# Optimization experiments

Measured on AMD Instinct MI355X. Metric: run time of the kernel, lower is better.

## Reference

```python
import jax, jax.numpy as jnp
import numpy as np

N, K, D_IN, D_H, D_A, N_CLS = 8192, 10, 1024, 512, 256, 4


def setup_inputs() -> dict:
    key = jax.random.key(0)
    ks = jax.random.split(key, 20)
    def lin(k, fan_in, shape):
        return jax.random.normal(k, shape, dtype=jnp.float32) / np.sqrt(fan_in)
    return {
        "x_path": jax.random.normal(ks[0], (N, D_IN), dtype=jnp.float32),
        "cluster_id": jax.random.randint(ks[1], (N,), 0, K),
        # per-cluster phi MLP (Linear 1024->512, ReLU, Linear 512->512, ReLU); dropout = eval identity
        "W1": lin(ks[2], D_IN, (K, D_IN, D_H)), "b1": jnp.zeros((K, D_H), jnp.float32),
        "W2": lin(ks[3], D_H, (K, D_H, D_H)), "b2": jnp.zeros((K, D_H), jnp.float32),
        # attention_net fc: Linear 512->512 + ReLU
        "fc_W": lin(ks[4], D_H, (D_H, D_H)), "fc_b": jnp.zeros((D_H,), jnp.float32),
        # Attn_Net_Gated: a=tanh(Va), b=sigmoid(Vb), A=(a*b)@Vc
        "Va": lin(ks[5], D_H, (D_H, D_A)), "ba": jnp.zeros((D_A,), jnp.float32),
        "Vb": lin(ks[6], D_H, (D_H, D_A)), "bb": jnp.zeros((D_A,), jnp.float32),
        "Vc": lin(ks[7], D_A, (D_A, 1)), "bc": jnp.zeros((1,), jnp.float32),
        # rho: Linear 512->256 + ReLU
        "rho_W": lin(ks[8], D_H, (D_H, D_A)), "rho_b": jnp.zeros((D_A,), jnp.float32),
        # classifier: Linear 256->4
        "cls_W": lin(ks[9], D_A, (D_A, N_CLS)), "cls_b": jnp.zeros((N_CLS,), jnp.float32),
    }


def reference(x_path, cluster_id, W1, b1, W2, b2, fc_W, fc_b,
              Va, ba, Vb, bb, Vc, bc, rho_W, rho_b, cls_W, cls_b):
    # mask[k, n] = 1 if patch n belongs to cluster k
    mask = (cluster_id[None, :] == jnp.arange(K)[:, None]).astype(x_path.dtype)  # [K, N]

    # per-cluster 2-layer MLP applied to all patches, masked mean-pool (= AdaptiveAvgPool1d(1))
    def phi(W1i, b1i, W2i, b2i):
        h = jax.nn.relu(x_path @ W1i + b1i)          # [N, 512]
        return jax.nn.relu(h @ W2i + b2i)            # [N, 512]
    y = jax.vmap(phi)(W1, b1, W2, b2)                # [K, N, 512]
    cnt = mask.sum(axis=1)                           # [K]
    pooled = jnp.einsum('kn,knd->kd', mask, y) / jnp.maximum(cnt, 1.0)[:, None]  # [K, 512]
    # empty cluster -> zeros (matches torch.zeros((1,512)) branch since b terms are zero via where)
    pooled = jnp.where(cnt[:, None] > 0, pooled, 0.0)

    # attention_net: fc + gated attention
    h = jax.nn.relu(pooled @ fc_W + fc_b)            # [K, 512]
    a = jnp.tanh(h @ Va + ba)                        # [K, 256]
    b = jax.nn.sigmoid(h @ Vb + bb)                  # [K, 256]
    A = (a * b) @ Vc + bc                            # [K, 1]
    A = jax.nn.softmax(A.T, axis=1)                  # [1, K]
    h_path = A @ h                                   # [1, 512]
    h_path = jax.nn.relu(h_path @ rho_W + rho_b)[0]  # [256]
    logits = (h_path @ cls_W + cls_b)[None, :]       # [1, 4]
    Y_hat = jnp.argmax(logits, axis=1, keepdims=True)
    hazards = jax.nn.sigmoid(logits)
    S = jnp.cumprod(1.0 - hazards, axis=1)
    return hazards, S, Y_hat
```

## Files before the change

kernel.cpp:

```cpp
#include <hip/hip_runtime.h>
#include <math.h>

#define NPATCH 8192
#define KC     10
#define DIN    1024
#define DH     512
#define DA     256
#define NCLS   4

#define TM  32
#define LDA 520

typedef unsigned short u16;
typedef short bf16x8 __attribute__((ext_vector_type(8)));
typedef float f32x4  __attribute__((ext_vector_type(4)));

#define OFF_CNT   0
#define OFF_IDX   64
#define OFF_PSUM  327744
#define OFF_H     348224
#define OFF_S     368704
#define OFF_H2    368768
#define OFF_W1P   369792
#define OFF_W2P   10855552
#define OFF_XB    16098432
#define OFF_H1    32875648

__device__ __forceinline__ u16 f2bf(float f) {
  union { float f; unsigned u; } v; v.f = f;
  unsigned r = (v.u + 0x7fffu + ((v.u >> 16) & 1u)) >> 16;
  return (u16)r;
}

struct __align__(8) U16x4 { u16 x, y, z, w; };

__device__ __forceinline__ void async16(const void* gp, void* lp) {
  __builtin_amdgcn_global_load_lds(
      (const __attribute__((address_space(1))) void*)gp,
      (__attribute__((address_space(3))) void*)lp, 16, 0, 0);
}

#define W1_TILES (KC * (DIN / 32) * (DH / 32))
#define W2_TILES (KC * (DH / 32) * (DH / 32))
#define NB_BUCKET 32
#define NB_XB     2048
#define NB_PREP   (NB_BUCKET + W1_TILES + W2_TILES + NB_XB)

__global__ __launch_bounds__(256) void prep_kernel(
    const int* __restrict__ cid, int* __restrict__ cnt,
    int* __restrict__ idxlist, const float* __restrict__ W1,
    const float* __restrict__ W2, u16* __restrict__ W1p,
    u16* __restrict__ W2p, const float* __restrict__ x,
    u16* __restrict__ xb, float* __restrict__ psum,
    float* __restrict__ sstore) {
  int b = blockIdx.x, t = threadIdx.x;
  if (b < NB_BUCKET) {
    int g = b * 256 + t;
    if (g < KC * DH) psum[g] = 0.f;
    if (g < KC) sstore[g] = 0.f;
    __shared__ int lcnt[KC], lbase[KC];
    if (t < KC) lcnt[t] = 0;
    __syncthreads();
    int n = b * 256 + t;
    int k = cid[n];
    int myoff = atomicAdd(&lcnt[k], 1);
    __syncthreads();
    if (t < KC) lbase[t] = atomicAdd(&cnt[t], lcnt[t]);
    __syncthreads();
    idxlist[k * NPATCH + lbase[k] + myoff] = n;
  } else if (b < NB_BUCKET + W1_TILES + W2_TILES) {
    __shared__ u16 tile[32][33];
    int bb = b - NB_BUCKET;
    const float* src;
    u16* dst;
    if (bb < W1_TILES) {
      int k = bb / 512, rem = bb % 512;
      int kb = rem / 16, n0 = (rem % 16) * 32;
      src = W1 + (size_t)k * DIN * DH + (size_t)kb * 32 * DH + n0;
      dst = W1p + (((size_t)(k * 32 + kb) * 512 + n0) * 32);
    } else {
      int b2 = bb - W1_TILES;
      int k = b2 / 256, rem = b2 % 256;
      int kb = rem / 16, n0 = (rem % 16) * 32;
      src = W2 + (size_t)k * DH * DH + (size_t)kb * 32 * DH + n0;
      dst = W2p + (((size_t)(k * 16 + kb) * 512 + n0) * 32);
    }
    {
      int ki = t >> 3, n4 = (t & 7) * 4;
      float4 v = *(const float4*)&src[(size_t)ki * DH + n4];
      tile[ki][n4 + 0] = f2bf(v.x);
      tile[ki][n4 + 1] = f2bf(v.y);
      tile[ki][n4 + 2] = f2bf(v.z);
      tile[ki][n4 + 3] = f2bf(v.w);
    }
    __syncthreads();
    {
      int n = t >> 3, ki = (t & 7) * 4;
      U16x4 o = {tile[ki + 0][n], tile[ki + 1][n], tile[ki + 2][n],
                 tile[ki + 3][n]};
      *(U16x4*)&dst[(size_t)n * 32 + ki] = o;
    }
  } else {
    int cb = b - (NB_BUCKET + W1_TILES + W2_TILES);
    size_t basei = (size_t)cb * 4096;
#pragma unroll
    for (int i = 0; i < 4; ++i) {
      size_t off = basei + (size_t)i * 1024 + (size_t)t * 4;
      float4 v = *(const float4*)(x + off);
      U16x4 o = {f2bf(v.x), f2bf(v.y), f2bf(v.z), f2bf(v.w)};
      *(U16x4*)(xb + off) = o;
    }
  }
}

__global__ __launch_bounds__(256) void phi1_kernel(
    const u16* __restrict__ xb, const u16* __restrict__ W1p,
    const float* __restrict__ b1, const int* __restrict__ cnt,
    const int* __restrict__ idxlist, u16* __restrict__ h1) {
  const int k = blockIdx.y;
  const int base = blockIdx.x * TM;
  const int nq = blockIdx.z;
  const int cntk = cnt[k];
  if (base >= cntk) return;

  const int tid = threadIdx.x;
  const int w = tid >> 6, lane = tid & 63;
  const int quad = lane >> 4, l16 = lane & 15;

  __shared__ __align__(16) u16 A_sh[TM * LDA];
  __shared__ int ridx[TM];
  if (tid < TM) {
    int r = base + tid;
    ridx[tid] = (r < cntk) ? idxlist[k * NPATCH + r] : -1;
  }
  __syncthreads();

  const f32x4 zero4 = {0.f, 0.f, 0.f, 0.f};
  f32x4 acc[2][2];
#pragma unroll
  for (int m = 0; m < 2; ++m)
#pragma unroll
    for (int nt = 0; nt < 2; ++nt) acc[m][nt] = zero4;

  for (int kh = 0; kh < 2; ++kh) {
    if (kh) __syncthreads();
    for (int rr = 0; rr < 8; ++rr) {
      int r = w * 8 + rr;
      int src = ridx[r];
      if (src >= 0) {
        async16(xb + (size_t)src * DIN + kh * 512 + lane * 8, &A_sh[r * LDA]);
      } else {
        bf16x8 z = {0, 0, 0, 0, 0, 0, 0, 0};
        *(bf16x8*)&A_sh[r * LDA + lane * 8] = z;
      }
    }
    __syncthreads();

    const u16* wb = W1p + ((size_t)(k * 32 + kh * 16) * 512 +
                           (nq * 128 + w * 32 + l16)) * 32 + quad * 8;
    bf16x8 B[2][8];
#pragma unroll
    for (int s = 0; s < 4; ++s)
#pragma unroll
      for (int nt = 0; nt < 2; ++nt)
        B[0][s * 2 + nt] = *(const bf16x8*)(wb + (size_t)s * 16384 + nt * 512);
#pragma unroll
    for (int g = 0; g < 4; ++g) {
      const int cur = g & 1, nxt = cur ^ 1;
      if (g < 3) {
#pragma unroll
        for (int s = 0; s < 4; ++s)
#pragma unroll
          for (int nt = 0; nt < 2; ++nt)
            B[nxt][s * 2 + nt] = *(const bf16x8*)(
                wb + (size_t)((g + 1) * 4 + s) * 16384 + nt * 512);
      }
#pragma unroll
      for (int s = 0; s < 4; ++s) {
        const int ks = g * 4 + s;
        bf16x8 af0 = *(const bf16x8*)&A_sh[l16 * LDA + ks * 32 + quad * 8];
        bf16x8 af1 =
            *(const bf16x8*)&A_sh[(16 + l16) * LDA + ks * 32 + quad * 8];
#pragma unroll
        for (int nt = 0; nt < 2; ++nt) {
          acc[0][nt] = __builtin_amdgcn_mfma_f32_16x16x32_bf16(
              af0, B[cur][s * 2 + nt], acc[0][nt], 0, 0, 0);
          acc[1][nt] = __builtin_amdgcn_mfma_f32_16x16x32_bf16(
              af1, B[cur][s * 2 + nt], acc[1][nt], 0, 0, 0);
        }
      }
    }
  }

  __syncthreads();
#pragma unroll
  for (int m = 0; m < 2; ++m)
#pragma unroll
    for (int nt = 0; nt < 2; ++nt) {
      int c = w * 32 + nt * 16 + l16;
      float bias = b1[k * DH + nq * 128 + c];
#pragma unroll
      for (int r = 0; r < 4; ++r) {
        int row = m * 16 + quad * 4 + r;
        A_sh[row * 136 + c] = f2bf(fmaxf(acc[m][nt][r] + bias, 0.f));
      }
    }
  __syncthreads();
  {
    int row = tid >> 3, seg = tid & 7;
    int n = ridx[row];
    if (n >= 0) {
      u16* dst = h1 + (size_t)n * DH + nq * 128 + seg * 16;
#pragma unroll
      for (int j = 0; j < 2; ++j)
        *(bf16x8*)(dst + j * 8) =
            *(const bf16x8*)&A_sh[row * 136 + seg * 16 + j * 8];
    }
  }
}

__global__ __launch_bounds__(256) void phi2_kernel(
    const u16* __restrict__ h1, const u16* __restrict__ W2p,
    const float* __restrict__ b2, const int* __restrict__ cnt,
    const int* __restrict__ idxlist, float* __restrict__ psum) {
  const int k = blockIdx.y;
  const int base = blockIdx.x * TM;
  const int nq = blockIdx.z;
  const int cntk = cnt[k];
  if (base >= cntk) return;

  const int tid = threadIdx.x;
  const int w = tid >> 6, lane = tid & 63;
  const int quad = lane >> 4, l16 = lane & 15;

  __shared__ __align__(16) u16 H_sh[TM * LDA];
  __shared__ int ridx[TM];
  if (tid < TM) {
    int r = base + tid;
    ridx[tid] = (r < cntk) ? idxlist[k * NPATCH + r] : -1;
  }
  __syncthreads();

  for (int rr = 0; rr < 8; ++rr) {
    int r = w * 8 + rr;
    int src = ridx[r];
    if (src >= 0) {
      async16(h1 + (size_t)src * DH + lane * 8, &H_sh[r * LDA]);
    } else {
      bf16x8 z = {0, 0, 0, 0, 0, 0, 0, 0};
      *(bf16x8*)&H_sh[r * LDA + lane * 8] = z;
    }
  }
  __syncthreads();

  const f32x4 zero4 = {0.f, 0.f, 0.f, 0.f};
  f32x4 acc[2][2];
#pragma unroll
  for (int m = 0; m < 2; ++m)
#pragma unroll
    for (int nt = 0; nt < 2; ++nt) acc[m][nt] = zero4;

  const u16* wb = W2p + ((size_t)(k * 16) * 512 +
                         (nq * 128 + w * 32 + l16)) * 32 + quad * 8;
  bf16x8 B[2][8];
#pragma unroll
  for (int s = 0; s < 4; ++s)
#pragma unroll
    for (int nt = 0; nt < 2; ++nt)
      B[0][s * 2 + nt] = *(const bf16x8*)(wb + (size_t)s * 16384 + nt * 512);
#pragma unroll
  for (int g = 0; g < 4; ++g) {
    const int cur = g & 1, nxt = cur ^ 1;
    if (g < 3) {
#pragma unroll
      for (int s = 0; s < 4; ++s)
#pragma unroll
        for (int nt = 0; nt < 2; ++nt)
          B[nxt][s * 2 + nt] = *(const bf16x8*)(
              wb + (size_t)((g + 1) * 4 + s) * 16384 + nt * 512);
    }
#pragma unroll
    for (int s = 0; s < 4; ++s) {
      const int ks = g * 4 + s;
      bf16x8 af0 = *(const bf16x8*)&H_sh[l16 * LDA + ks * 32 + quad * 8];
      bf16x8 af1 =
          *(const bf16x8*)&H_sh[(16 + l16) * LDA + ks * 32 + quad * 8];
#pragma unroll
      for (int nt = 0; nt < 2; ++nt) {
        acc[0][nt] = __builtin_amdgcn_mfma_f32_16x16x32_bf16(
            af0, B[cur][s * 2 + nt], acc[0][nt], 0, 0, 0);
        acc[1][nt] = __builtin_amdgcn_mfma_f32_16x16x32_bf16(
            af1, B[cur][s * 2 + nt], acc[1][nt], 0, 0, 0);
      }
    }
  }

  float vmask[2][4];
#pragma unroll
  for (int m = 0; m < 2; ++m)
#pragma unroll
    for (int r = 0; r < 4; ++r)
      vmask[m][r] = (ridx[m * 16 + quad * 4 + r] >= 0) ? 1.f : 0.f;

#pragma unroll
  for (int nt = 0; nt < 2; ++nt) {
    int col = nq * 128 + w * 32 + nt * 16 + l16;
    float bias = b2[k * DH + col];
    float s = 0.f;
#pragma unroll
    for (int m = 0; m < 2; ++m)
#pragma unroll
      for (int r = 0; r < 4; ++r)
        s += vmask[m][r] * fmaxf(acc[m][nt][r] + bias, 0.f);
    s += __shfl_xor(s, 16, 64);
    s += __shfl_xor(s, 32, 64);
    if (quad == 0) atomicAdd(&psum[k * DH + col], s);
  }
}

__global__ __launch_bounds__(256) void fc_kernel(
    const float* __restrict__ psum, const int* __restrict__ cnt,
    const float* __restrict__ fcW, const float* __restrict__ fcb,
    float* __restrict__ hstore) {
  __shared__ float p_sh[KC * DH];
  __shared__ float invs[16];
  __shared__ float red[16 * 16 * KC];
  const int tid = threadIdx.x;
  const int j0 = blockIdx.x * 16;
  const int j = tid & 15, dq = tid >> 4;

  if (tid < KC) {
    int c = cnt[tid];
    invs[tid] = (c > 0) ? 1.f / (float)c : 0.f;
  }
  __syncthreads();
#pragma unroll
  for (int it = 0; it < KC * DH / 256; ++it) {
    int e = it * 256 + tid;
    p_sh[e] = psum[e] * invs[e >> 9];
  }
  __syncthreads();

  float acc[KC];
#pragma unroll
  for (int k = 0; k < KC; ++k) acc[k] = 0.f;
#pragma unroll 8
  for (int i = 0; i < 32; ++i) {
    int ii = (i + dq) & 31;
    int d = dq * 32 + ii;
    float wv = fcW[(size_t)d * DH + j0 + j];
#pragma unroll
    for (int k = 0; k < KC; ++k)
      acc[k] = fmaf(p_sh[k * DH + d], wv, acc[k]);
  }
#pragma unroll
  for (int k = 0; k < KC; ++k) red[(dq * 16 + j) * KC + k] = acc[k];
  __syncthreads();
  if (tid < 16 * KC) {
    int jj = tid / KC, k = tid % KC;
    float s = 0.f;
#pragma unroll
    for (int q = 0; q < 16; ++q) s += red[(q * 16 + jj) * KC + k];
    hstore[k * DH + j0 + jj] = fmaxf(s + fcb[j0 + jj], 0.f);
  }
}

__global__ __launch_bounds__(256) void attn_kernel(
    const float* __restrict__ hstore, const float* __restrict__ Va,
    const float* __restrict__ ba, const float* __restrict__ Vb,
    const float* __restrict__ bb_, const float* __restrict__ Vc,
    float* __restrict__ sstore) {
  __shared__ float h_sh[KC * DH];
  __shared__ float reda[16 * 16 * KC];
  __shared__ float redb[16 * 16 * KC];
  __shared__ float gred[16 * KC];
  const int tid = threadIdx.x;
  const int j0 = blockIdx.x * 16;
  const int j = tid & 15, dq = tid >> 4;

#pragma unroll
  for (int it = 0; it < KC * DH / 256; ++it) {
    int e = it * 256 + tid;
    h_sh[e] = hstore[e];
  }
  __syncthreads();

  float sa[KC], sb[KC];
#pragma unroll
  for (int k = 0; k < KC; ++k) { sa[k] = 0.f; sb[k] = 0.f; }
#pragma unroll 8
  for (int i = 0; i < 32; ++i) {
    int ii = (i + dq) & 31;
    int d = dq * 32 + ii;
    float va = Va[(size_t)d * DA + j0 + j];
    float vb = Vb[(size_t)d * DA + j0 + j];
#pragma unroll
    for (int k = 0; k < KC; ++k) {
      float h = h_sh[k * DH + d];
      sa[k] = fmaf(h, va, sa[k]);
      sb[k] = fmaf(h, vb, sb[k]);
    }
  }
#pragma unroll
  for (int k = 0; k < KC; ++k) {
    reda[(dq * 16 + j) * KC + k] = sa[k];
    redb[(dq * 16 + j) * KC + k] = sb[k];
  }
  __syncthreads();
  if (tid < 16 * KC) {
    int jj = tid / KC, k = tid % KC;
    float ta = 0.f, tb = 0.f;
#pragma unroll
    for (int q = 0; q < 16; ++q) {
      ta += reda[(q * 16 + jj) * KC + k];
      tb += redb[(q * 16 + jj) * KC + k];
    }
    float a = tanhf(ta + ba[j0 + jj]);
    float b = 1.f / (1.f + expf(-(tb + bb_[j0 + jj])));
    gred[jj * KC + k] = a * b * Vc[j0 + jj];
  }
  __syncthreads();
  if (tid < KC) {
    float s = 0.f;
#pragma unroll
    for (int jj = 0; jj < 16; ++jj) s += gred[jj * KC + tid];
    atomicAdd(&sstore[tid], s);
  }
}

__global__ __launch_bounds__(256) void rho_kernel(
    const float* __restrict__ hstore, const float* __restrict__ sstore,
    const float* __restrict__ rhoW, const float* __restrict__ rhob,
    float* __restrict__ h2g) {
  __shared__ float ws_sh[KC];
  __shared__ float hp_sh[DH];
  __shared__ float red[8 * 32];
  const int tid = threadIdx.x;
  const int j0 = blockIdx.x * 32;
  const int j = tid & 31, dq = tid >> 5;

  if (tid == 0) {
    float sv[KC], m = -1e30f;
#pragma unroll
    for (int k = 0; k < KC; ++k) { sv[k] = sstore[k]; m = fmaxf(m, sv[k]); }
    float Z = 0.f;
#pragma unroll
    for (int k = 0; k < KC; ++k) { sv[k] = expf(sv[k] - m); Z += sv[k]; }
    float invZ = 1.f / Z;
#pragma unroll
    for (int k = 0; k < KC; ++k) ws_sh[k] = sv[k] * invZ;
  }
  __syncthreads();
#pragma unroll
  for (int it = 0; it < 2; ++it) {
    int d = it * 256 + tid;
    float s = 0.f;
#pragma unroll
    for (int k = 0; k < KC; ++k) s = fmaf(ws_sh[k], hstore[k * DH + d], s);
    hp_sh[d] = s;
  }
  __syncthreads();

  float acc = 0.f;
#pragma unroll 8
  for (int i = 0; i < 64; ++i) {
    int d = dq * 64 + i;
    acc = fmaf(hp_sh[d], rhoW[(size_t)d * DA + j0 + j], acc);
  }
  red[dq * 32 + j] = acc;
  __syncthreads();
  if (tid < 32) {
    float s = 0.f;
#pragma unroll
    for (int q = 0; q < 8; ++q) s += red[q * 32 + tid];
    h2g[j0 + tid] = fmaxf(s + rhob[j0 + tid], 0.f);
  }
}

__global__ __launch_bounds__(256) void cls_kernel(
    const float* __restrict__ h2g, const float* __restrict__ clsW,
    const float* __restrict__ clsb, float* __restrict__ out) {
  __shared__ float rd[NCLS][256];
  const int tid = threadIdx.x;
  float h = h2g[tid];
#pragma unroll
  for (int c = 0; c < NCLS; ++c) rd[c][tid] = h * clsW[tid * NCLS + c];
  __syncthreads();
  for (int s = 128; s > 0; s >>= 1) {
    if (tid < s) {
#pragma unroll
      for (int c = 0; c < NCLS; ++c) rd[c][tid] += rd[c][tid + s];
    }
    __syncthreads();
  }
  if (tid == 0) {
    float lg[NCLS], hz[NCLS];
    int best = 0;
#pragma unroll
    for (int c = 0; c < NCLS; ++c) {
      lg[c] = rd[c][0] + clsb[c];
      hz[c] = 1.f / (1.f + expf(-lg[c]));
      if (lg[c] > lg[best]) best = c;
    }
    float S = 1.f;
#pragma unroll
    for (int c = 0; c < NCLS; ++c) out[c] = hz[c];
#pragma unroll
    for (int c = 0; c < NCLS; ++c) {
      S *= (1.f - hz[c]);
      out[NCLS + c] = S;
    }
    out[2 * NCLS] = (float)best;
  }
}

extern "C" void kernel_launch(void* const* d_in, const int* in_sizes, int n_in,
                              void* d_out, int out_size, void* d_ws,
                              size_t ws_size, hipStream_t stream) {
  const float* x    = (const float*)d_in[0];
  const int*   cid  = (const int*)d_in[1];
  const float* W1   = (const float*)d_in[2];
  const float* b1   = (const float*)d_in[3];
  const float* W2   = (const float*)d_in[4];
  const float* b2   = (const float*)d_in[5];
  const float* fcW  = (const float*)d_in[6];
  const float* fcb  = (const float*)d_in[7];
  const float* Va   = (const float*)d_in[8];
  const float* ba   = (const float*)d_in[9];
  const float* Vb   = (const float*)d_in[10];
  const float* bb_  = (const float*)d_in[11];
  const float* Vc   = (const float*)d_in[12];
  const float* rhoW = (const float*)d_in[14];
  const float* rhob = (const float*)d_in[15];
  const float* clsW = (const float*)d_in[16];
  const float* clsb = (const float*)d_in[17];
  float* out = (float*)d_out;

  char* ws = (char*)d_ws;
  int*   cnt     = (int*)(ws + OFF_CNT);
  int*   idxlist = (int*)(ws + OFF_IDX);
  float* psum    = (float*)(ws + OFF_PSUM);
  float* hstore  = (float*)(ws + OFF_H);
  float* sstore  = (float*)(ws + OFF_S);
  float* h2g     = (float*)(ws + OFF_H2);
  u16*   W1p     = (u16*)(ws + OFF_W1P);
  u16*   W2p     = (u16*)(ws + OFF_W2P);
  u16*   xb      = (u16*)(ws + OFF_XB);
  u16*   h1      = (u16*)(ws + OFF_H1);

  (void)hipMemsetAsync(cnt, 0, 64, stream);
  prep_kernel<<<NB_PREP, 256, 0, stream>>>(cid, cnt, idxlist, W1, W2, W1p, W2p,
                                           x, xb, psum, sstore);
  phi1_kernel<<<dim3(NPATCH / TM, KC, 4), 256, 0, stream>>>(xb, W1p, b1, cnt,
                                                            idxlist, h1);
  phi2_kernel<<<dim3(NPATCH / TM, KC, 4), 256, 0, stream>>>(h1, W2p, b2, cnt,
                                                            idxlist, psum);
  fc_kernel<<<32, 256, 0, stream>>>(psum, cnt, fcW, fcb, hstore);
  attn_kernel<<<16, 256, 0, stream>>>(hstore, Va, ba, Vb, bb_, Vc, sstore);
  rho_kernel<<<8, 256, 0, stream>>>(hstore, sstore, rhoW, rhob, h2g);
  cls_kernel<<<1, 256, 0, stream>>>(h2g, clsW, clsb, out);
}
```

Before: 202.2 us.

## Fuse x bf16 conversion into phi1 and merge head kernels with grid barriers

Removes the separate pass converting x to bf16; phi1 now loads fp32 rows of gathered patches and converts them to bf16 while staging into LDS. The four small tail kernels (fc, attention, rho, classifier) are merged into one 32-block kernel separated by atomic grid barriers. This targets the extra memory traffic of the conversion pass and the launch overhead of the tail kernels. The cost is that phi1 reads fp32 x (twice the bytes) once per column quarter and loses async LDS loads, and the spin barrier relies on all 32 blocks being co-resident.

```diff
diff --git a/kernel.cpp b/kernel.cpp
--- a/kernel.cpp
+++ b/kernel.cpp
@@ -16,6 +16,7 @@
 typedef float f32x4  __attribute__((ext_vector_type(4)));
 
 #define OFF_CNT   0
+#define OFF_BAR   40
 #define OFF_IDX   64
 #define OFF_PSUM  327744
 #define OFF_H     348224
@@ -23,8 +24,7 @@
 #define OFF_H2    368768
 #define OFF_W1P   369792
 #define OFF_W2P   10855552
-#define OFF_XB    16098432
-#define OFF_H1    32875648
+#define OFF_H1    16098432
 
 __device__ __forceinline__ u16 f2bf(float f) {
   union { float f; unsigned u; } v; v.f = f;
@@ -43,15 +43,13 @@
 #define W1_TILES (KC * (DIN / 32) * (DH / 32))
 #define W2_TILES (KC * (DH / 32) * (DH / 32))
 #define NB_BUCKET 32
-#define NB_XB     2048
-#define NB_PREP   (NB_BUCKET + W1_TILES + W2_TILES + NB_XB)
+#define NB_PREP   (NB_BUCKET + W1_TILES + W2_TILES)
 
 __global__ __launch_bounds__(256) void prep_kernel(
     const int* __restrict__ cid, int* __restrict__ cnt,
     int* __restrict__ idxlist, const float* __restrict__ W1,
     const float* __restrict__ W2, u16* __restrict__ W1p,
-    u16* __restrict__ W2p, const float* __restrict__ x,
-    u16* __restrict__ xb, float* __restrict__ psum,
+    u16* __restrict__ W2p, float* __restrict__ psum,
     float* __restrict__ sstore) {
   int b = blockIdx.x, t = threadIdx.x;
   if (b < NB_BUCKET) {
@@ -68,7 +66,7 @@
     if (t < KC) lbase[t] = atomicAdd(&cnt[t], lcnt[t]);
     __syncthreads();
     idxlist[k * NPATCH + lbase[k] + myoff] = n;
-  } else if (b < NB_BUCKET + W1_TILES + W2_TILES) {
+  } else {
     __shared__ u16 tile[32][33];
     int bb = b - NB_BUCKET;
     const float* src;
@@ -100,21 +98,11 @@
                  tile[ki + 3][n]};
       *(U16x4*)&dst[(size_t)n * 32 + ki] = o;
     }
-  } else {
-    int cb = b - (NB_BUCKET + W1_TILES + W2_TILES);
-    size_t basei = (size_t)cb * 4096;
-#pragma unroll
-    for (int i = 0; i < 4; ++i) {
-      size_t off = basei + (size_t)i * 1024 + (size_t)t * 4;
-      float4 v = *(const float4*)(x + off);
-      U16x4 o = {f2bf(v.x), f2bf(v.y), f2bf(v.z), f2bf(v.w)};
-      *(U16x4*)(xb + off) = o;
-    }
   }
 }
 
 __global__ __launch_bounds__(256) void phi1_kernel(
-    const u16* __restrict__ xb, const u16* __restrict__ W1p,
+    const float* __restrict__ x, const u16* __restrict__ W1p,
     const float* __restrict__ b1, const int* __restrict__ cnt,
     const int* __restrict__ idxlist, u16* __restrict__ h1) {
   const int k = blockIdx.y;
@@ -142,17 +130,25 @@
 #pragma unroll
     for (int nt = 0; nt < 2; ++nt) acc[m][nt] = zero4;
 
+  const int srow = tid >> 3;
+  const int sc0 = (tid & 7) * 4;
+  const int asrc = ridx[srow];
+
   for (int kh = 0; kh < 2; ++kh) {
     if (kh) __syncthreads();
-    for (int rr = 0; rr < 8; ++rr) {
-      int r = w * 8 + rr;
-      int src = ridx[r];
-      if (src >= 0) {
-        async16(xb + (size_t)src * DIN + kh * 512 + lane * 8, &A_sh[r * LDA]);
-      } else {
-        bf16x8 z = {0, 0, 0, 0, 0, 0, 0, 0};
-        *(bf16x8*)&A_sh[r * LDA + lane * 8] = z;
-      }
+    if (asrc >= 0) {
+      const float* xr = x + (size_t)asrc * DIN + kh * 512;
+#pragma unroll
+      for (int c = 0; c < 16; ++c) {
+        float4 v = *(const float4*)(xr + sc0 + c * 32);
+        U16x4 o = {f2bf(v.x), f2bf(v.y), f2bf(v.z), f2bf(v.w)};
+        *(U16x4*)&A_sh[srow * LDA + sc0 + c * 32] = o;
+      }
+    } else {
+      U16x4 o = {0, 0, 0, 0};
+#pragma unroll
+      for (int c = 0; c < 16; ++c)
+        *(U16x4*)&A_sh[srow * LDA + sc0 + c * 32] = o;
     }
     __syncthreads();
 
@@ -318,199 +314,210 @@
   }
 }
 
-__global__ __launch_bounds__(256) void fc_kernel(
+__device__ __forceinline__ void gsync(int* bar) {
+  __syncthreads();
+  if (threadIdx.x == 0) {
+    __threadfence();
+    atomicAdd(bar, 1);
+    while (__hip_atomic_load(bar, __ATOMIC_RELAXED,
+                             __HIP_MEMORY_SCOPE_AGENT) < 32) {
+      __builtin_amdgcn_s_sleep(1);
+    }
+    __threadfence();
+  }
+  __syncthreads();
+}
+
+__global__ __launch_bounds__(256) void head_kernel(
     const float* __restrict__ psum, const int* __restrict__ cnt,
     const float* __restrict__ fcW, const float* __restrict__ fcb,
-    float* __restrict__ hstore) {
-  __shared__ float p_sh[KC * DH];
-  __shared__ float invs[16];
-  __shared__ float red[16 * 16 * KC];
+    const float* __restrict__ Va, const float* __restrict__ ba,
+    const float* __restrict__ Vb, const float* __restrict__ bb_,
+    const float* __restrict__ Vc, const float* __restrict__ rhoW,
+    const float* __restrict__ rhob, const float* __restrict__ clsW,
+    const float* __restrict__ clsb, float* __restrict__ hstore,
+    float* __restrict__ sstore, float* __restrict__ h2g, int* __restrict__ bar,
+    float* __restrict__ out) {
+  __shared__ __align__(16) float smem[10496];
   const int tid = threadIdx.x;
-  const int j0 = blockIdx.x * 16;
-  const int j = tid & 15, dq = tid >> 4;
-
-  if (tid < KC) {
-    int c = cnt[tid];
-    invs[tid] = (c > 0) ? 1.f / (float)c : 0.f;
-  }
-  __syncthreads();
-#pragma unroll
-  for (int it = 0; it < KC * DH / 256; ++it) {
-    int e = it * 256 + tid;
-    p_sh[e] = psum[e] * invs[e >> 9];
-  }
-  __syncthreads();
-
-  float acc[KC];
-#pragma unroll
-  for (int k = 0; k < KC; ++k) acc[k] = 0.f;
+  const int blk = blockIdx.x;
+
+  {
+    float* p_sh = smem;
+    float* red = smem + 5120;
+    float* invs = smem + 7680;
+    const int j0 = blk * 16;
+    const int j = tid & 15, dq = tid >> 4;
+    if (tid < KC) {
+      int c = cnt[tid];
+      invs[tid] = (c > 0) ? 1.f / (float)c : 0.f;
+    }
+    __syncthreads();
+#pragma unroll
+    for (int it = 0; it < KC * DH / 256; ++it) {
+      int e = it * 256 + tid;
+      p_sh[e] = psum[e] * invs[e >> 9];
+    }
+    __syncthreads();
+    float acc[KC];
+#pragma unroll
+    for (int k = 0; k < KC; ++k) acc[k] = 0.f;
 #pragma unroll 8
-  for (int i = 0; i < 32; ++i) {
-    int ii = (i + dq) & 31;
-    int d = dq * 32 + ii;
-    float wv = fcW[(size_t)d * DH + j0 + j];
-#pragma unroll
-    for (int k = 0; k < KC; ++k)
-      acc[k] = fmaf(p_sh[k * DH + d], wv, acc[k]);
-  }
-#pragma unroll
-  for (int k = 0; k < KC; ++k) red[(dq * 16 + j) * KC + k] = acc[k];
-  __syncthreads();
-  if (tid < 16 * KC) {
-    int jj = tid / KC, k = tid % KC;
-    float s = 0.f;
-#pragma unroll
-    for (int q = 0; q < 16; ++q) s += red[(q * 16 + jj) * KC + k];
-    hstore[k * DH + j0 + jj] = fmaxf(s + fcb[j0 + jj], 0.f);
-  }
-}
-
-__global__ __launch_bounds__(256) void attn_kernel(
-    const float* __restrict__ hstore, const float* __restrict__ Va,
-    const float* __restrict__ ba, const float* __restrict__ Vb,
-    const float* __restrict__ bb_, const float* __restrict__ Vc,
-    float* __restrict__ sstore) {
-  __shared__ float h_sh[KC * DH];
-  __shared__ float reda[16 * 16 * KC];
-  __shared__ float redb[16 * 16 * KC];
-  __shared__ float gred[16 * KC];
-  const int tid = threadIdx.x;
-  const int j0 = blockIdx.x * 16;
-  const int j = tid & 15, dq = tid >> 4;
-
-#pragma unroll
-  for (int it = 0; it < KC * DH / 256; ++it) {
-    int e = it * 256 + tid;
-    h_sh[e] = hstore[e];
-  }
-  __syncthreads();
-
-  float sa[KC], sb[KC];
-#pragma unroll
-  for (int k = 0; k < KC; ++k) { sa[k] = 0.f; sb[k] = 0.f; }
+    for (int i = 0; i < 32; ++i) {
+      int ii = (i + dq) & 31;
+      int d = dq * 32 + ii;
+      float wv = fcW[(size_t)d * DH + j0 + j];
+#pragma unroll
+      for (int k = 0; k < KC; ++k)
+        acc[k] = fmaf(p_sh[k * DH + d], wv, acc[k]);
+    }
+#pragma unroll
+    for (int k = 0; k < KC; ++k) red[(dq * 16 + j) * KC + k] = acc[k];
+    __syncthreads();
+    if (tid < 16 * KC) {
+      int jj = tid / KC, k = tid % KC;
+      float s = 0.f;
+#pragma unroll
+      for (int q = 0; q < 16; ++q) s += red[(q * 16 + jj) * KC + k];
+      hstore[k * DH + j0 + jj] = fmaxf(s + fcb[j0 + jj], 0.f);
+    }
+  }
+  gsync(&bar[0]);
+
+  if (blk < 16) {
+    float* h_sh = smem;
+    float* reda = smem + 5120;
+    float* redb = smem + 7680;
+    float* gred = smem + 10240;
+    const int j0 = blk * 16;
+    const int j = tid & 15, dq = tid >> 4;
+#pragma unroll
+    for (int it = 0; it < KC * DH / 256; ++it) {
+      int e = it * 256 + tid;
+      h_sh[e] = hstore[e];
+    }
+    __syncthreads();
+    float sa[KC], sb[KC];
+#pragma unroll
+    for (int k = 0; k < KC; ++k) { sa[k] = 0.f; sb[k] = 0.f; }
 #pragma unroll 8
-  for (int i = 0; i < 32; ++i) {
-    int ii = (i + dq) & 31;
-    int d = dq * 32 + ii;
-    float va = Va[(size_t)d * DA + j0 + j];
-    float vb = Vb[(size_t)d * DA + j0 + j];
+    for (int i = 0; i < 32; ++i) {
+      int ii = (i + dq) & 31;
+      int d = dq * 32 + ii;
+      float va = Va[(size_t)d * DA + j0 + j];
+      float vb = Vb[(size_t)d * DA + j0 + j];
+#pragma unroll
+      for (int k = 0; k < KC; ++k) {
+        float h = h_sh[k * DH + d];
+        sa[k] = fmaf(h, va, sa[k]);
+        sb[k] = fmaf(h, vb, sb[k]);
+      }
+    }
 #pragma unroll
     for (int k = 0; k < KC; ++k) {
-      float h = h_sh[k * DH + d];
-      sa[k] = fmaf(h, va, sa[k]);
-      sb[k] = fmaf(h, vb, sb[k]);
-    }
-  }
-#pragma unroll
-  for (int k = 0; k < KC; ++k) {
-    reda[(dq * 16 + j) * KC + k] = sa[k];
-    redb[(dq * 16 + j) * KC + k] = sb[k];
-  }
-  __syncthreads();
-  if (tid < 16 * KC) {
-    int jj = tid / KC, k = tid % KC;
-    float ta = 0.f, tb = 0.f;
-#pragma unroll
-    for (int q = 0; q < 16; ++q) {
-      ta += reda[(q * 16 + jj) * KC + k];
-      tb += redb[(q * 16 + jj) * KC + k];
-    }
-    float a = tanhf(ta + ba[j0 + jj]);
-    float b = 1.f / (1.f + expf(-(tb + bb_[j0 + jj])));
-    gred[jj * KC + k] = a * b * Vc[j0 + jj];
-  }
-  __syncthreads();
-  if (tid < KC) {
-    float s = 0.f;
-#pragma unroll
-    for (int jj = 0; jj < 16; ++jj) s += gred[jj * KC + tid];
-    atomicAdd(&sstore[tid], s);
-  }
-}
-
-__global__ __launch_bounds__(256) void rho_kernel(
-    const float* __restrict__ hstore, const float* __restrict__ sstore,
-    const float* __restrict__ rhoW, const float* __restrict__ rhob,
-    float* __restrict__ h2g) {
-  __shared__ float ws_sh[KC];
-  __shared__ float hp_sh[DH];
-  __shared__ float red[8 * 32];
-  const int tid = threadIdx.x;
-  const int j0 = blockIdx.x * 32;
-  const int j = tid & 31, dq = tid >> 5;
-
-  if (tid == 0) {
-    float sv[KC], m = -1e30f;
-#pragma unroll
-    for (int k = 0; k < KC; ++k) { sv[k] = sstore[k]; m = fmaxf(m, sv[k]); }
-    float Z = 0.f;
-#pragma unroll
-    for (int k = 0; k < KC; ++k) { sv[k] = expf(sv[k] - m); Z += sv[k]; }
-    float invZ = 1.f / Z;
-#pragma unroll
-    for (int k = 0; k < KC; ++k) ws_sh[k] = sv[k] * invZ;
-  }
-  __syncthreads();
-#pragma unroll
-  for (int it = 0; it < 2; ++it) {
-    int d = it * 256 + tid;
-    float s = 0.f;
-#pragma unroll
-    for (int k = 0; k < KC; ++k) s = fmaf(ws_sh[k], hstore[k * DH + d], s);
-    hp_sh[d] = s;
-  }
-  __syncthreads();
-
-  float acc = 0.f;
+      reda[(dq * 16 + j) * KC + k] = sa[k];
+      redb[(dq * 16 + j) * KC + k] = sb[k];
+    }
+    __syncthreads();
+    if (tid < 16 * KC) {
+      int jj = tid / KC, k = tid % KC;
+      float ta = 0.f, tb = 0.f;
+#pragma unroll
+      for (int q = 0; q < 16; ++q) {
+        ta += reda[(q * 16 + jj) * KC + k];
+        tb += redb[(q * 16 + jj) * KC + k];
+      }
+      float a = tanhf(ta + ba[j0 + jj]);
+      float b = 1.f / (1.f + expf(-(tb + bb_[j0 + jj])));
+      gred[jj * KC + k] = a * b * Vc[j0 + jj];
+    }
+    __syncthreads();
+    if (tid < KC) {
+      float s = 0.f;
+#pragma unroll
+      for (int jj = 0; jj < 16; ++jj) s += gred[jj * KC + tid];
+      atomicAdd(&sstore[tid], s);
+    }
+  }
+  gsync(&bar[1]);
+
+  if (blk < 8) {
+    float* ws_sh = smem;
+    float* hp_sh = smem + 64;
+    float* red = smem + 1024;
+    const int j0 = blk * 32;
+    const int j = tid & 31, dq = tid >> 5;
+    if (tid == 0) {
+      float sv[KC], m = -1e30f;
+#pragma unroll
+      for (int k = 0; k < KC; ++k) { sv[k] = sstore[k]; m = fmaxf(m, sv[k]); }
+      float Z = 0.f;
+#pragma unroll
+      for (int k = 0; k < KC; ++k) { sv[k] = expf(sv[k] - m); Z += sv[k]; }
+      float invZ = 1.f / Z;
+#pragma unroll
+      for (int k = 0; k < KC; ++k) ws_sh[k] = sv[k] * invZ;
+    }
+    __syncthreads();
+#pragma unroll
+    for (int it = 0; it < 2; ++it) {
+      int d = it * 256 + tid;
+      float s = 0.f;
+#pragma unroll
+      for (int k = 0; k < KC; ++k) s = fmaf(ws_sh[k], hstore[k * DH + d], s);
+      hp_sh[d] = s;
+    }
+    __syncthreads();
+    float acc = 0.f;
 #pragma unroll 8
-  for (int i = 0; i < 64; ++i) {
-    int d = dq * 64 + i;
-    acc = fmaf(hp_sh[d], rhoW[(size_t)d * DA + j0 + j], acc);
-  }
-  red[dq * 32 + j] = acc;
-  __syncthreads();
-  if (tid < 32) {
-    float s = 0.f;
-#pragma unroll
-    for (int q = 0; q < 8; ++q) s += red[q * 32 + tid];
-    h2g[j0 + tid] = fmaxf(s + rhob[j0 + tid], 0.f);
-  }
-}
-
-__global__ __launch_bounds__(256) void cls_kernel(
-    const float* __restrict__ h2g, const float* __restrict__ clsW,
-    const float* __restrict__ clsb, float* __restrict__ out) {
-  __shared__ float rd[NCLS][256];
-  const int tid = threadIdx.x;
-  float h = h2g[tid];
-#pragma unroll
-  for (int c = 0; c < NCLS; ++c) rd[c][tid] = h * clsW[tid * NCLS + c];
-  __syncthreads();
-  for (int s = 128; s > 0; s >>= 1) {
-    if (tid < s) {
-#pragma unroll
-      for (int c = 0; c < NCLS; ++c) rd[c][tid] += rd[c][tid + s];
-    }
-    __syncthreads();
-  }
-  if (tid == 0) {
-    float lg[NCLS], hz[NCLS];
-    int best = 0;
-#pragma unroll
-    for (int c = 0; c < NCLS; ++c) {
-      lg[c] = rd[c][0] + clsb[c];
-      hz[c] = 1.f / (1.f + expf(-lg[c]));
-      if (lg[c] > lg[best]) best = c;
-    }
-    float S = 1.f;
-#pragma unroll
-    for (int c = 0; c < NCLS; ++c) out[c] = hz[c];
-#pragma unroll
-    for (int c = 0; c < NCLS; ++c) {
-      S *= (1.f - hz[c]);
-      out[NCLS + c] = S;
-    }
-    out[2 * NCLS] = (float)best;
+    for (int i = 0; i < 64; ++i) {
+      int d = dq * 64 + i;
+      acc = fmaf(hp_sh[d], rhoW[(size_t)d * DA + j0 + j], acc);
+    }
+    red[dq * 32 + j] = acc;
+    __syncthreads();
+    if (tid < 32) {
+      float s = 0.f;
+#pragma unroll
+      for (int q = 0; q < 8; ++q) s += red[q * 32 + tid];
+      h2g[j0 + tid] = fmaxf(s + rhob[j0 + tid], 0.f);
+    }
+  }
+  gsync(&bar[2]);
+
+  if (blk == 0) {
+    float* rd = smem;
+    float h = h2g[tid];
+#pragma unroll
+    for (int c = 0; c < NCLS; ++c) rd[c * 256 + tid] = h * clsW[tid * NCLS + c];
+    __syncthreads();
+    for (int s = 128; s > 0; s >>= 1) {
+      if (tid < s) {
+#pragma unroll
+        for (int c = 0; c < NCLS; ++c)
+          rd[c * 256 + tid] += rd[c * 256 + tid + s];
+      }
+      __syncthreads();
+    }
+    if (tid == 0) {
+      float lg[NCLS], hz[NCLS];
+      int best = 0;
+#pragma unroll
+      for (int c = 0; c < NCLS; ++c) {
+        lg[c] = rd[c * 256] + clsb[c];
+        hz[c] = 1.f / (1.f + expf(-lg[c]));
+        if (lg[c] > lg[best]) best = c;
+      }
+      float S = 1.f;
+#pragma unroll
+      for (int c = 0; c < NCLS; ++c) out[c] = hz[c];
+#pragma unroll
+      for (int c = 0; c < NCLS; ++c) {
+        S *= (1.f - hz[c]);
+        out[NCLS + c] = S;
+      }
+      out[2 * NCLS] = (float)best;
+    }
   }
 }
 
@@ -538,6 +545,7 @@
 
   char* ws = (char*)d_ws;
   int*   cnt     = (int*)(ws + OFF_CNT);
+  int*   bar     = (int*)(ws + OFF_BAR);
   int*   idxlist = (int*)(ws + OFF_IDX);
   float* psum    = (float*)(ws + OFF_PSUM);
   float* hstore  = (float*)(ws + OFF_H);
@@ -545,18 +553,16 @@
   float* h2g     = (float*)(ws + OFF_H2);
   u16*   W1p     = (u16*)(ws + OFF_W1P);
   u16*   W2p     = (u16*)(ws + OFF_W2P);
-  u16*   xb      = (u16*)(ws + OFF_XB);
   u16*   h1      = (u16*)(ws + OFF_H1);
 
   (void)hipMemsetAsync(cnt, 0, 64, stream);
   prep_kernel<<<NB_PREP, 256, 0, stream>>>(cid, cnt, idxlist, W1, W2, W1p, W2p,
-                                           x, xb, psum, sstore);
-  phi1_kernel<<<dim3(NPATCH / TM, KC, 4), 256, 0, stream>>>(xb, W1p, b1, cnt,
+                                           psum, sstore);
+  phi1_kernel<<<dim3(NPATCH / TM, KC, 4), 256, 0, stream>>>(x, W1p, b1, cnt,
                                                             idxlist, h1);
   phi2_kernel<<<dim3(NPATCH / TM, KC, 4), 256, 0, stream>>>(h1, W2p, b2, cnt,
                                                             idxlist, psum);
-  fc_kernel<<<32, 256, 0, stream>>>(psum, cnt, fcW, fcb, hstore);
-  attn_kernel<<<16, 256, 0, stream>>>(hstore, Va, ba, Vb, bb_, Vc, sstore);
-  rho_kernel<<<8, 256, 0, stream>>>(hstore, sstore, rhoW, rhob, h2g);
-  cls_kernel<<<1, 256, 0, stream>>>(h2g, clsW, clsb, out);
-}
+  head_kernel<<<32, 256, 0, stream>>>(psum, cnt, fcW, fcb, Va, ba, Vb, bb_, Vc,
+                                      rhoW, rhob, clsW, clsb, hstore, sstore,
+                                      h2g, bar, out);
+}
```

Result: slower. 207.5 us (+2.6%).
